# Performance work log

Measured on AMD Instinct MI355X. Metric: run time of the kernel, lower is better.

Reference implementation:

```python
import jax, jax.numpy as jnp
import numpy as np

DIM, ORDER, HID = 512, 2, 64
B, S = 4, 8192


def setup_inputs() -> dict:
    key = jax.random.key(0)
    ks = jax.random.split(key, 16)
    rnd = lambda k, shape, scale: (jax.random.normal(k, shape, dtype=jnp.float32) * scale)
    return {
        'x': rnd(ks[0], (B, S, DIM), 1.0),
        # ImplicitFilter MLP: Linear(1,64) -> GELU -> Linear(64,64) -> GELU -> Linear(64,dim)
        'w1': rnd(ks[1], (1, HID), 1.0),
        'b1': rnd(ks[2], (HID,), 0.02),
        'w2': rnd(ks[3], (HID, HID), 1.0 / np.sqrt(HID)),
        'b2': rnd(ks[4], (HID,), 0.02),
        'w3': rnd(ks[5], (HID, DIM), 1.0 / np.sqrt(HID)),
        'b3': rnd(ks[6], (DIM,), 0.02),
        # depthwise Conv1d(dim, dim, k=3, padding=1, groups=dim): weight (dim, 3)
        'conv_w': rnd(ks[7], (DIM, 3), 1.0 / np.sqrt(3)),
        'conv_b': rnd(ks[8], (DIM,), 0.02),
        # in_proj: Linear(dim, dim*(order+1))
        'w_in': rnd(ks[9], (DIM, DIM * (ORDER + 1)), 1.0 / np.sqrt(DIM)),
        'b_in': rnd(ks[10], (DIM * (ORDER + 1),), 0.02),
        # out_proj: Linear(dim, dim)
        'w_out': rnd(ks[11], (DIM, DIM), 1.0 / np.sqrt(DIM)),
        'b_out': rnd(ks[12], (DIM,), 0.02),
    }


def _gelu(x):
    return jax.nn.gelu(x, approximate=False)  # torch nn.GELU default is exact erf


def reference(x, w1, b1, w2, b2, w3, b3, conv_w, conv_b, w_in, b_in, w_out, b_out):
    batch, seq_len, dim = x.shape
    # in_proj and split into order+1 paths
    proj = x @ w_in + b_in                      # (B, S, 3D)
    v, u, z = jnp.split(proj, 3, axis=-1)       # each (B, S, D)
    # implicit filter from positions
    pos = jnp.linspace(0.0, 1.0, seq_len, dtype=x.dtype)[:, None]   # (S, 1)
    filt = _gelu(_gelu(pos @ w1 + b1) @ w2 + b2) @ w3 + b3          # (S, D)
    # depthwise short conv, kernel=3, padding=1 (cross-correlation as in torch)
    up = jnp.pad(u, ((0, 0), (1, 1), (0, 0)))
    u_short = (up[:, :-2] * conv_w[:, 0] + up[:, 1:-1] * conv_w[:, 1]
               + up[:, 2:] * conv_w[:, 2] + conv_b)                 # (B, S, D)
    # FFT long convolution (circular, matching torch rfft/irfft with n=seq_len)
    U = jnp.fft.rfft(u_short, axis=1)                               # (B, S//2+1, D)
    F = jnp.fft.rfft(filt, n=seq_len, axis=0)[None]                 # (1, S//2+1, D)
    filtered = jnp.fft.irfft(U * F, n=seq_len, axis=1)              # (B, S, D)
    # multiplicative gates
    out = v * filtered * jax.nn.sigmoid(z)
    return out @ w_out + b_out
```

## Files before the change

### kernel.cpp

```cpp
#include <hip/hip_runtime.h>
#include <math.h>

#define DIM   512
#define NB    4
#define NS    8192
#define FFT_N 8192
#define FT    1024
#define MTOT  (NB*NS)

#define IDX(i) ((i) + ((i) >> 3))
#define XSZ   9216

typedef __attribute__((ext_vector_type(8))) short bf16x8;
typedef __attribute__((ext_vector_type(4))) short short4v;
typedef __attribute__((ext_vector_type(8))) short short8v;
typedef __attribute__((ext_vector_type(4))) float f32x4;

__device__ __forceinline__ float bf2f(unsigned short u) {
    union { unsigned int i; float f; } v; v.i = ((unsigned int)u) << 16; return v.f;
}
__device__ __forceinline__ unsigned short f2bf(float f) {
    union { float f; unsigned int i; } v; v.f = f;
    unsigned int r = v.i + 0x7fffu + ((v.i >> 16) & 1u);
    return (unsigned short)(r >> 16);
}
__device__ __forceinline__ float2 cmulf(float2 a, float2 b) {
    return make_float2(a.x*b.x - a.y*b.y, a.x*b.y + a.y*b.x);
}
__device__ __forceinline__ float2 cadd(float2 a, float2 b) { return make_float2(a.x+b.x, a.y+b.y); }
__device__ __forceinline__ float2 csub(float2 a, float2 b) { return make_float2(a.x-b.x, a.y-b.y); }
__device__ __forceinline__ float gelu_exact(float x) {
    return 0.5f * x * (1.0f + erff(x * 0.70710678118654752f));
}
__device__ __forceinline__ void gload16(const void* g, void* l) {
    __builtin_amdgcn_global_load_lds((const __attribute__((address_space(1))) void*)g,
                                     (__attribute__((address_space(3))) void*)l, 16, 0, 0);
}

__global__ void filter_mlp_kernel(const float* __restrict__ w1, const float* __restrict__ b1,
                                  const float* __restrict__ w2, const float* __restrict__ b2,
                                  const float* __restrict__ w3, const float* __restrict__ b3,
                                  float* __restrict__ filt) {
    __shared__ float h1[64];
    __shared__ float h2[64];
    const int s = blockIdx.x;
    const int t = threadIdx.x;
    const float pos = (float)s / (float)(NS - 1);
    h1[t] = gelu_exact(pos * w1[t] + b1[t]);
    __syncthreads();
    float acc = b2[t];
    #pragma unroll 8
    for (int j = 0; j < 64; ++j) acc += h1[j] * w2[j*64 + t];
    h2[t] = gelu_exact(acc);
    __syncthreads();
    for (int d = t; d < DIM; d += 64) {
        float o = b3[d];
        #pragma unroll 8
        for (int j = 0; j < 64; ++j) o += h2[j] * w3[j*DIM + d];
        filt[(size_t)s*DIM + d] = o;
    }
}

__global__ void transpose_f32_kernel(const float* __restrict__ in, float* __restrict__ out,
                                     int R, int C) {
    __shared__ float tile[64][65];
    const int c0 = blockIdx.x * 64, r0 = blockIdx.y * 64;
    const int t = threadIdx.x;
    const int rr = t >> 4, c4 = (t & 15) * 4;
    #pragma unroll
    for (int p = 0; p < 4; ++p) {
        const int r = rr + p*16;
        float4 v = *(const float4*)&in[(size_t)(r0 + r)*C + c0 + c4];
        tile[r][c4+0]=v.x; tile[r][c4+1]=v.y; tile[r][c4+2]=v.z; tile[r][c4+3]=v.w;
    }
    __syncthreads();
    const int cc = t >> 4, r4 = (t & 15) * 4;
    #pragma unroll
    for (int p = 0; p < 4; ++p) {
        const int c = cc + p*16;
        float4 o = make_float4(tile[r4+0][c], tile[r4+1][c], tile[r4+2][c], tile[r4+3][c]);
        *(float4*)&out[(size_t)(c0 + c)*R + r0 + r4] = o;
    }
}

__global__ void castT_kernel(const float* __restrict__ in, unsigned short* __restrict__ outT,
                             int R, int C) {
    __shared__ float tile[64][65];
    const int c0 = blockIdx.x * 64, r0 = blockIdx.y * 64;
    const int t = threadIdx.x;
    const int rr = t >> 4, c4 = (t & 15) * 4;
    #pragma unroll
    for (int p = 0; p < 4; ++p) {
        const int r = rr + p*16;
        float4 v = *(const float4*)&in[(size_t)(r0 + r)*C + c0 + c4];
        tile[r][c4+0]=v.x; tile[r][c4+1]=v.y; tile[r][c4+2]=v.z; tile[r][c4+3]=v.w;
    }
    __syncthreads();
    const int cc = t >> 4, r4 = (t & 15) * 4;
    #pragma unroll
    for (int p = 0; p < 4; ++p) {
        const int c = cc + p*16;
        short4v o;
        o[0] = (short)f2bf(tile[r4+0][c]); o[1] = (short)f2bf(tile[r4+1][c]);
        o[2] = (short)f2bf(tile[r4+2][c]); o[3] = (short)f2bf(tile[r4+3][c]);
        *(short4v*)&outT[(size_t)(c0 + c)*R + r0 + r4] = o;
    }
}

__global__ void cast_x_kernel(const float* __restrict__ in, unsigned short* __restrict__ out) {
    const size_t i = ((size_t)blockIdx.x * 256 + threadIdx.x) * 8;
    float4 a = *(const float4*)&in[i];
    float4 b = *(const float4*)&in[i+4];
    short8v o;
    o[0]=(short)f2bf(a.x); o[1]=(short)f2bf(a.y); o[2]=(short)f2bf(a.z); o[3]=(short)f2bf(a.w);
    o[4]=(short)f2bf(b.x); o[5]=(short)f2bf(b.y); o[6]=(short)f2bf(b.z); o[7]=(short)f2bf(b.w);
    *(short8v*)&out[i] = o;
}

template<int LOGQ>
__device__ __forceinline__ void dif4_stage(float2* X) {
    const int q = 1 << LOGQ;
    const float step = -6.28318530717958647692f / (float)(4*q);
    #pragma unroll
    for (int it = 0; it < (FFT_N/4)/FT; ++it) {
        const int idx = threadIdx.x + it*FT;
        const int g = idx >> LOGQ, k = idx & (q-1);
        const int base = (g << (LOGQ+2)) + k;
        const int i0 = IDX(base), i1 = IDX(base+q), i2 = IDX(base+2*q), i3 = IDX(base+3*q);
        float2 a=X[i0], b=X[i1], c=X[i2], d=X[i3];
        float2 t0=cadd(a,c), t1=csub(a,c), t2=cadd(b,d), t3=csub(b,d);
        float2 y0=cadd(t0,t2), y2=csub(t0,t2);
        float2 y1=make_float2(t1.x+t3.y, t1.y-t3.x);
        float2 y3=make_float2(t1.x-t3.y, t1.y+t3.x);
        float sv, cv; __sincosf(step*(float)k, &sv, &cv);
        float2 w1=make_float2(cv, sv);
        float2 w2=cmulf(w1, w1);
        float2 w3=cmulf(w2, w1);
        X[i0] = y0;
        X[i1] = cmulf(y1, w1);
        X[i2] = cmulf(y2, w2);
        X[i3] = cmulf(y3, w3);
    }
    __syncthreads();
}

template<int LOGQ>
__device__ __forceinline__ void dit4_stage_inv(float2* X) {
    const int q = 1 << LOGQ;
    const float step = 6.28318530717958647692f / (float)(4*q);
    #pragma unroll
    for (int it = 0; it < (FFT_N/4)/FT; ++it) {
        const int idx = threadIdx.x + it*FT;
        const int g = idx >> LOGQ, k = idx & (q-1);
        const int base = (g << (LOGQ+2)) + k;
        const int i0 = IDX(base), i1 = IDX(base+q), i2 = IDX(base+2*q), i3 = IDX(base+3*q);
        float sv, cv; __sincosf(step*(float)k, &sv, &cv);
        float2 w1=make_float2(cv, sv);
        float2 w2=cmulf(w1, w1);
        float2 w3=cmulf(w2, w1);
        float2 u0=X[i0];
        float2 u1=cmulf(X[i1], w1);
        float2 u2=cmulf(X[i2], w2);
        float2 u3=cmulf(X[i3], w3);
        float2 s02=cadd(u0,u2), d02=csub(u0,u2);
        float2 s13=cadd(u1,u3), d13=csub(u1,u3);
        X[i0] = cadd(s02, s13);
        X[i2] = csub(s02, s13);
        X[i1] = make_float2(d02.x - d13.y, d02.y + d13.x);
        X[i3] = make_float2(d02.x + d13.y, d02.y - d13.x);
    }
    __syncthreads();
}

__device__ __forceinline__ void reg_fwd(float2* E) {
    const float C = 0.70710678118654752f;
    {
        float2 t0=cadd(E[0],E[4]), t1=csub(E[0],E[4]);
        float2 t2=cadd(E[2],E[6]), t3=csub(E[2],E[6]);
        E[0]=cadd(t0,t2);
        E[4]=csub(t0,t2);
        E[2]=make_float2(t1.x+t3.y, t1.y-t3.x);
        E[6]=make_float2(t1.x-t3.y, t1.y+t3.x);
    }
    {
        float2 t0=cadd(E[1],E[5]), t1=csub(E[1],E[5]);
        float2 t2=cadd(E[3],E[7]), t3=csub(E[3],E[7]);
        float2 y0=cadd(t0,t2), y2=csub(t0,t2);
        float2 y1=make_float2(t1.x+t3.y, t1.y-t3.x);
        float2 y3=make_float2(t1.x-t3.y, t1.y+t3.x);
        E[1]=y0;
        E[3]=make_float2(C*(y1.x+y1.y),  C*(y1.y-y1.x));
        E[5]=make_float2(y2.y, -y2.x);
        E[7]=make_float2(C*(y3.y-y3.x), -C*(y3.x+y3.y));
    }
    #pragma unroll
    for (int j = 0; j < 8; j += 2) {
        float2 a=E[j], b=E[j+1];
        E[j]=cadd(a,b); E[j+1]=csub(a,b);
    }
}
__device__ __forceinline__ void reg_inv(float2* E) {
    const float C = 0.70710678118654752f;
    #pragma unroll
    for (int j = 0; j < 8; j += 2) {
        float2 a=E[j], b=E[j+1];
        E[j]=cadd(a,b); E[j+1]=csub(a,b);
    }
    {
        float2 u0=E[0], u1=E[2], u2=E[4], u3=E[6];
        float2 s02=cadd(u0,u2), d02=csub(u0,u2);
        float2 s13=cadd(u1,u3), d13=csub(u1,u3);
        E[0]=cadd(s02,s13);
        E[4]=csub(s02,s13);
        E[2]=make_float2(d02.x - d13.y, d02.y + d13.x);
        E[6]=make_float2(d02.x + d13.y, d02.y - d13.x);
    }
    {
        float2 z1=E[3], z2=E[5], z3=E[7];
        float2 u0=E[1];
        float2 u1=make_float2(C*(z1.x - z1.y), C*(z1.x + z1.y));
        float2 u2=make_float2(-z2.y, z2.x);
        float2 u3=make_float2(-C*(z3.x + z3.y), C*(z3.x - z3.y));
        float2 s02=cadd(u0,u2), d02=csub(u0,u2);
        float2 s13=cadd(u1,u3), d13=csub(u1,u3);
        E[1]=cadd(s02,s13);
        E[5]=csub(s02,s13);
        E[3]=make_float2(d02.x - d13.y, d02.y + d13.x);
        E[7]=make_float2(d02.x + d13.y, d02.y - d13.x);
    }
}

__device__ __forceinline__ void load8p(const float2* X, int t, float2* E) {
    const float2* b = X + 9*t;
    #pragma unroll
    for (int j = 0; j < 8; ++j) E[j] = b[j];
}
__device__ __forceinline__ void store8p(float2* X, int t, const float2* E) {
    float2* b = X + 9*t;
    #pragma unroll
    for (int j = 0; j < 8; ++j) b[j] = E[j];
}

__global__ __launch_bounds__(FT)
void fft_filt_kernel(const float* __restrict__ filtT, float2* __restrict__ Fbr) {
    __shared__ float2 X[XSZ];
    const int dd = blockIdx.x;
    const int t = threadIdx.x;
    const float* f = filtT + (size_t)dd * FFT_N;
    {
        float4 a = *(const float4*)(f + 8*t);
        float4 b = *(const float4*)(f + 8*t + 4);
        float2 E[8];
        E[0]=make_float2(a.x,0.f); E[1]=make_float2(a.y,0.f);
        E[2]=make_float2(a.z,0.f); E[3]=make_float2(a.w,0.f);
        E[4]=make_float2(b.x,0.f); E[5]=make_float2(b.y,0.f);
        E[6]=make_float2(b.z,0.f); E[7]=make_float2(b.w,0.f);
        store8p(X, t, E);
    }
    __syncthreads();
    dif4_stage<11>(X);
    dif4_stage<9>(X);
    dif4_stage<7>(X);
    dif4_stage<5>(X);
    dif4_stage<3>(X);
    {
        float2 E[8];
        load8p(X, t, E);
        reg_fwd(E);
        float2* o = Fbr + (size_t)dd*FFT_N + 8*t;
        #pragma unroll
        for (int j = 0; j < 8; ++j) o[j] = E[j];
    }
}

__global__ __launch_bounds__(FT)
void fft_conv_kernel(unsigned short* __restrict__ uT, const float2* __restrict__ Fbr) {
    __shared__ float2 X[XSZ];
    const int d = blockIdx.x & (DIM - 1);
    const int p = blockIdx.x >> 9;
    unsigned short* u1 = uT + (size_t)((2*p    )*DIM + d) * FFT_N;
    unsigned short* u2 = uT + (size_t)((2*p + 1)*DIM + d) * FFT_N;
    const int t = threadIdx.x;
    {
        short8v a = *(const short8v*)(u1 + 8*t);
        short8v b = *(const short8v*)(u2 + 8*t);
        float2 E[8];
        #pragma unroll
        for (int j = 0; j < 8; ++j)
            E[j] = make_float2(bf2f((unsigned short)a[j]), bf2f((unsigned short)b[j]));
        store8p(X, t, E);
    }
    __syncthreads();
    dif4_stage<11>(X);
    dif4_stage<9>(X);
    dif4_stage<7>(X);
    dif4_stage<5>(X);
    dif4_stage<3>(X);
    {
        float2 E[8];
        load8p(X, t, E);
        reg_fwd(E);
        const float2* F = Fbr + (size_t)d*FFT_N + 8*t;
        #pragma unroll
        for (int j = 0; j < 8; ++j) E[j] = cmulf(E[j], F[j]);
        reg_inv(E);
        store8p(X, t, E);
    }
    __syncthreads();
    dit4_stage_inv<3>(X);
    dit4_stage_inv<5>(X);
    dit4_stage_inv<7>(X);
    dit4_stage_inv<9>(X);
    dit4_stage_inv<11>(X);
    {
        float2 E[8];
        load8p(X, t, E);
        const float sc = 1.0f / (float)FFT_N;
        short8v a, b;
        #pragma unroll
        for (int j = 0; j < 8; ++j) {
            a[j] = (short)f2bf(E[j].x * sc);
            b[j] = (short)f2bf(E[j].y * sc);
        }
        *(short8v*)(u1 + 8*t) = a;
        *(short8v*)(u2 + 8*t) = b;
    }
}

__global__ void conv_transpose_kernel(const unsigned short* __restrict__ u,
                                      const float* __restrict__ conv_w,
                                      const float* __restrict__ conv_b,
                                      unsigned short* __restrict__ uT) {
    __shared__ float tile[66][65];
    const int bid = blockIdx.x;
    const int dt = bid & 7, st = (bid >> 3) & 127, b = bid >> 10;
    const int d0 = dt*64, s0 = st*64;
    const int t = threadIdx.x;
    const int rr = t >> 4, c4 = (t & 15) * 4;
    for (int r = rr; r < 66; r += 16) {
        const int s = s0 + r - 1;
        float v0=0.f, v1=0.f, v2=0.f, v3=0.f;
        if (s >= 0 && s < NS) {
            short4v xv = *(const short4v*)&u[((size_t)(b*NS + s))*DIM + d0 + c4];
            v0=bf2f((unsigned short)xv[0]); v1=bf2f((unsigned short)xv[1]);
            v2=bf2f((unsigned short)xv[2]); v3=bf2f((unsigned short)xv[3]);
        }
        tile[r][c4]=v0; tile[r][c4+1]=v1; tile[r][c4+2]=v2; tile[r][c4+3]=v3;
    }
    __syncthreads();
    const int dl = t >> 4, s4 = (t & 15) * 4;
    #pragma unroll
    for (int p = 0; p < 4; ++p) {
        const int dc = dl + p*16;
        const int d = d0 + dc;
        const float w0 = conv_w[d*3], w1 = conv_w[d*3+1], w2 = conv_w[d*3+2];
        const float cb = conv_b[d];
        short4v o;
        #pragma unroll
        for (int j = 0; j < 4; ++j) {
            const int sx = s4 + j;
            const float val = tile[sx][dc]*w0 + tile[sx+1][dc]*w1 + tile[sx+2][dc]*w2 + cb;
            o[j] = (short)f2bf(val);
        }
        *(short4v*)&uT[((size_t)(b*DIM + d))*FFT_N + s0 + s4] = o;
    }
}

template<int MODE>
__global__ __launch_bounds__(256)
void gemm_bt_kernel(const unsigned short* __restrict__ A,
                    const unsigned short* __restrict__ BT,
                    const float* __restrict__ bias,
                    float* __restrict__ Cf,
                    unsigned short* __restrict__ Cb) {
    __shared__ unsigned short As[2][4096];
    __shared__ unsigned short Bs[2][4096];
    const int tid = threadIdx.x;
    const int wid = tid >> 6, lane = tid & 63;
    const int bid = blockIdx.y * 4 + blockIdx.x;
    const int swz = (bid & 7) * 128 + (bid >> 3);
    const int m0 = (swz >> 2) * 128, n0 = (swz & 3) * 128;
    const int srow = wid*16 + (lane >> 2);
    const int scol = (lane & 3) * 8;
    const unsigned short* gA = A  + (size_t)(m0 + srow)*DIM + scol;
    const unsigned short* gB = BT + (size_t)(n0 + srow)*DIM + scol;
    const int wr = wid >> 1, wc = wid & 1;
    const int fr = lane & 15, fq = lane >> 4;
    f32x4 acc[4][4] = {};
    gload16(gA,                  &As[0][wid*512]);
    gload16(gA + (size_t)64*DIM, &As[0][wid*512 + 2048]);
    gload16(gB,                  &Bs[0][wid*512]);
    gload16(gB + (size_t)64*DIM, &Bs[0][wid*512 + 2048]);
    int cur = 0;
    for (int k0 = 0; k0 < DIM; k0 += 32) {
        __syncthreads();
        if (k0 + 32 < DIM) {
            const int nx = cur ^ 1;
            gload16(gA + k0 + 32,                  &As[nx][wid*512]);
            gload16(gA + k0 + 32 + (size_t)64*DIM, &As[nx][wid*512 + 2048]);
            gload16(gB + k0 + 32,                  &Bs[nx][wid*512]);
            gload16(gB + k0 + 32 + (size_t)64*DIM, &Bs[nx][wid*512 + 2048]);
        }
        bf16x8 af[4], bfr[4];
        #pragma unroll
        for (int mi = 0; mi < 4; ++mi)
            af[mi] = *(const bf16x8*)&As[cur][(wr*64 + mi*16 + fr)*32 + fq*8];
        #pragma unroll
        for (int ni = 0; ni < 4; ++ni)
            bfr[ni] = *(const bf16x8*)&Bs[cur][(wc*64 + ni*16 + fr)*32 + fq*8];
        #pragma unroll
        for (int mi = 0; mi < 4; ++mi)
            #pragma unroll
            for (int ni = 0; ni < 4; ++ni)
                acc[mi][ni] = __builtin_amdgcn_mfma_f32_16x16x32_bf16(af[mi], bfr[ni], acc[mi][ni], 0, 0, 0);
        cur ^= 1;
    }
    #pragma unroll
    for (int ni = 0; ni < 4; ++ni) {
        const int c = n0 + wc*64 + ni*16 + fr;
        const float bv = bias[c];
        #pragma unroll
        for (int mi = 0; mi < 4; ++mi) {
            const int rbase = m0 + wr*64 + mi*16 + fq*4;
            #pragma unroll
            for (int j = 0; j < 4; ++j) {
                const size_t idx = (size_t)(rbase + j)*DIM + c;
                const float val = acc[mi][ni][j] + bv;
                if (MODE == 0) Cb[idx] = f2bf(val);
                else           Cf[idx] = val;
            }
        }
    }
}

__global__ __launch_bounds__(256)
void gemm_vzg_kernel(const unsigned short* __restrict__ A,
                     const unsigned short* __restrict__ BT,
                     const float* __restrict__ bias,
                     const unsigned short* __restrict__ yT,
                     unsigned short* __restrict__ Cb) {
    __shared__ unsigned short As[2][4096];
    __shared__ unsigned short Bv[2][4096];
    __shared__ unsigned short Bz[2][4096];
    const int tid = threadIdx.x;
    const int wid = tid >> 6, lane = tid & 63;
    const int bid = blockIdx.y * 4 + blockIdx.x;
    const int swz = (bid & 7) * 128 + (bid >> 3);
    const int m0 = (swz >> 2) * 128, n0 = (swz & 3) * 128;
    const int srow = wid*16 + (lane >> 2);
    const int scol = (lane & 3) * 8;
    const unsigned short* gA  = A  + (size_t)(m0 + srow)*DIM + scol;
    const unsigned short* gBv = BT + (size_t)(n0 + srow)*DIM + scol;
    const unsigned short* gBz = BT + (size_t)(1024 + n0 + srow)*DIM + scol;
    const int wr = wid >> 1, wc = wid & 1;
    const int fr = lane & 15, fq = lane >> 4;
    f32x4 accv[4][4] = {};
    f32x4 accz[4][4] = {};
    gload16(gA,                   &As[0][wid*512]);
    gload16(gA  + (size_t)64*DIM, &As[0][wid*512 + 2048]);
    gload16(gBv,                  &Bv[0][wid*512]);
    gload16(gBv + (size_t)64*DIM, &Bv[0][wid*512 + 2048]);
    gload16(gBz,                  &Bz[0][wid*512]);
    gload16(gBz + (size_t)64*DIM, &Bz[0][wid*512 + 2048]);
    int cur = 0;
    for (int k0 = 0; k0 < DIM; k0 += 32) {
        __syncthreads();
        if (k0 + 32 < DIM) {
            const int nx = cur ^ 1;
            gload16(gA  + k0 + 32,                  &As[nx][wid*512]);
            gload16(gA  + k0 + 32 + (size_t)64*DIM, &As[nx][wid*512 + 2048]);
            gload16(gBv + k0 + 32,                  &Bv[nx][wid*512]);
            gload16(gBv + k0 + 32 + (size_t)64*DIM, &Bv[nx][wid*512 + 2048]);
            gload16(gBz + k0 + 32,                  &Bz[nx][wid*512]);
            gload16(gBz + k0 + 32 + (size_t)64*DIM, &Bz[nx][wid*512 + 2048]);
        }
        bf16x8 af[4], bf_[4];
        #pragma unroll
        for (int mi = 0; mi < 4; ++mi)
            af[mi] = *(const bf16x8*)&As[cur][(wr*64 + mi*16 + fr)*32 + fq*8];
        #pragma unroll
        for (int ni = 0; ni < 4; ++ni)
            bf_[ni] = *(const bf16x8*)&Bv[cur][(wc*64 + ni*16 + fr)*32 + fq*8];
        #pragma unroll
        for (int mi = 0; mi < 4; ++mi)
            #pragma unroll
            for (int ni = 0; ni < 4; ++ni)
                accv[mi][ni] = __builtin_amdgcn_mfma_f32_16x16x32_bf16(af[mi], bf_[ni], accv[mi][ni], 0, 0, 0);
        #pragma unroll
        for (int ni = 0; ni < 4; ++ni)
            bf_[ni] = *(const bf16x8*)&Bz[cur][(wc*64 + ni*16 + fr)*32 + fq*8];
        #pragma unroll
        for (int mi = 0; mi < 4; ++mi)
            #pragma unroll
            for (int ni = 0; ni < 4; ++ni)
                accz[mi][ni] = __builtin_amdgcn_mfma_f32_16x16x32_bf16(af[mi], bf_[ni], accz[mi][ni], 0, 0, 0);
        cur ^= 1;
    }
    const int b    = m0 >> 13;
    const int srel = (m0 & (NS-1)) + wr*64;
    #pragma unroll
    for (int ni = 0; ni < 4; ++ni) {
        const int c = n0 + wc*64 + ni*16 + fr;
        const float bv = bias[c];
        const float bz = bias[1024 + c];
        const unsigned short* yrow = yT + ((size_t)(b*DIM + c))*FFT_N + srel;
        #pragma unroll
        for (int mi = 0; mi < 4; ++mi) {
            const short4v yv = *(const short4v*)&yrow[mi*16 + fq*4];
            const int rbase = m0 + wr*64 + mi*16 + fq*4;
            #pragma unroll
            for (int j = 0; j < 4; ++j) {
                const size_t idx = (size_t)(rbase + j)*DIM + c;
                const float vv = accv[mi][ni][j] + bv;
                const float zz = accz[mi][ni][j] + bz;
                const float sg = 1.0f / (1.0f + __expf(-zz));
                const float yf = bf2f((unsigned short)yv[j]);
                Cb[idx] = f2bf(vv * sg * yf);
            }
        }
    }
}

extern "C" void kernel_launch(void* const* d_in, const int* in_sizes, int n_in,
                              void* d_out, int out_size, void* d_ws, size_t ws_size,
                              hipStream_t stream) {
    const float* x      = (const float*)d_in[0];
    const float* w1     = (const float*)d_in[1];
    const float* b1     = (const float*)d_in[2];
    const float* w2     = (const float*)d_in[3];
    const float* b2     = (const float*)d_in[4];
    const float* w3     = (const float*)d_in[5];
    const float* b3     = (const float*)d_in[6];
    const float* conv_w = (const float*)d_in[7];
    const float* conv_b = (const float*)d_in[8];
    const float* w_in   = (const float*)d_in[9];
    const float* b_in   = (const float*)d_in[10];
    const float* w_out  = (const float*)d_in[11];
    const float* b_out  = (const float*)d_in[12];
    float* out = (float*)d_out;

    const size_t NEED = 167772160ULL;
    if (ws_size < NEED) return;
    char* ws = (char*)d_ws;
    float2*         Fbr    = (float2*)ws;
    unsigned short* xb     = (unsigned short*)(ws + (size_t)( 32<<20));
    unsigned short* W2     = (unsigned short*)(ws + (size_t)( 64<<20));
    unsigned short* W3     = (unsigned short*)(ws + (size_t)( 96<<20));
    char*           W4     = ws + (size_t)(128<<20);
    float*          filt   = (float*)W4;
    float*          filtT  = (float*)(ws + (size_t)(96<<20));
    unsigned short* w_inT  = (unsigned short*)W4;
    unsigned short* w_outT = (unsigned short*)(W4 + (size_t)(2<<20));

    filter_mlp_kernel<<<NS, 64, 0, stream>>>(w1, b1, w2, b2, w3, b3, filt);
    transpose_f32_kernel<<<dim3(DIM/64, NS/64), 256, 0, stream>>>(filt, filtT, NS, DIM);
    fft_filt_kernel<<<DIM, FT, 0, stream>>>(filtT, Fbr);
    cast_x_kernel<<<(MTOT*DIM/8)/256, 256, 0, stream>>>(x, xb);
    castT_kernel<<<dim3(1536/64, DIM/64), 256, 0, stream>>>(w_in, w_inT, DIM, 1536);
    castT_kernel<<<dim3(DIM/64, DIM/64), 256, 0, stream>>>(w_out, w_outT, DIM, DIM);
    gemm_bt_kernel<0><<<dim3(4, MTOT/128), 256, 0, stream>>>(xb, w_inT + 512*DIM, b_in + 512, nullptr, W2);
    conv_transpose_kernel<<<NB*(NS/64)*(DIM/64), 256, 0, stream>>>(W2, conv_w, conv_b, W3);
    fft_conv_kernel<<<(NB/2)*DIM, FT, 0, stream>>>(W3, Fbr);
    gemm_vzg_kernel<<<dim3(4, MTOT/128), 256, 0, stream>>>(xb, w_inT, b_in, W3, W2);
    gemm_bt_kernel<2><<<dim3(4, MTOT/128), 256, 0, stream>>>(W2, w_outT, b_out, out, nullptr);
}
```

Measured before the change: 269.1 us.

## Compute v, u, z projections in one GEMM and apply FFT gate separately

```diff
diff --git a/kernel.cpp b/kernel.cpp
--- a/kernel.cpp
+++ b/kernel.cpp
@@ -363,6 +363,35 @@
             o[j] = (short)f2bf(val);
         }
         *(short4v*)&uT[((size_t)(b*DIM + d))*FFT_N + s0 + s4] = o;
+    }
+}
+
+__global__ void gate_kernel(unsigned short* __restrict__ vg, const unsigned short* __restrict__ yT) {
+    __shared__ float tile[64][65];
+    const int bid = blockIdx.x;
+    const int dt = bid & 7, st = (bid >> 3) & 127, b = bid >> 10;
+    const int d0 = dt*64, s0 = st*64;
+    const int t = threadIdx.x;
+    const int dl = t >> 4, s4 = (t & 15) * 4;
+    #pragma unroll
+    for (int p = 0; p < 4; ++p) {
+        const int d = dl + p*16;
+        short4v y = *(const short4v*)&yT[((size_t)(b*DIM + d0 + d))*FFT_N + s0 + s4];
+        tile[d][s4]  =bf2f((unsigned short)y[0]); tile[d][s4+1]=bf2f((unsigned short)y[1]);
+        tile[d][s4+2]=bf2f((unsigned short)y[2]); tile[d][s4+3]=bf2f((unsigned short)y[3]);
+    }
+    __syncthreads();
+    const int sl = t >> 4, d4 = (t & 15) * 4;
+    #pragma unroll
+    for (int p = 0; p < 4; ++p) {
+        const int s = s0 + sl + p*16;
+        unsigned short* pv = &vg[((size_t)(b*NS + s))*DIM + d0 + d4];
+        short4v v = *(short4v*)pv;
+        short4v o;
+        #pragma unroll
+        for (int j = 0; j < 4; ++j)
+            o[j] = (short)f2bf(bf2f((unsigned short)v[j]) * tile[d4+j][sl + p*16]);
+        *(short4v*)pv = o;
     }
 }
 
@@ -434,13 +463,14 @@
 }
 
 __global__ __launch_bounds__(256)
-void gemm_vzg_kernel(const unsigned short* __restrict__ A,
+void gemm_vzu_kernel(const unsigned short* __restrict__ A,
                      const unsigned short* __restrict__ BT,
                      const float* __restrict__ bias,
-                     const unsigned short* __restrict__ yT,
-                     unsigned short* __restrict__ Cb) {
+                     unsigned short* __restrict__ Gb,
+                     unsigned short* __restrict__ Ub) {
     __shared__ unsigned short As[2][4096];
     __shared__ unsigned short Bv[2][4096];
+    __shared__ unsigned short Bu[2][4096];
     __shared__ unsigned short Bz[2][4096];
     const int tid = threadIdx.x;
     const int wid = tid >> 6, lane = tid & 63;
@@ -451,15 +481,19 @@
     const int scol = (lane & 3) * 8;
     const unsigned short* gA  = A  + (size_t)(m0 + srow)*DIM + scol;
     const unsigned short* gBv = BT + (size_t)(n0 + srow)*DIM + scol;
+    const unsigned short* gBu = BT + (size_t)(512  + n0 + srow)*DIM + scol;
     const unsigned short* gBz = BT + (size_t)(1024 + n0 + srow)*DIM + scol;
     const int wr = wid >> 1, wc = wid & 1;
     const int fr = lane & 15, fq = lane >> 4;
     f32x4 accv[4][4] = {};
+    f32x4 accu[4][4] = {};
     f32x4 accz[4][4] = {};
     gload16(gA,                   &As[0][wid*512]);
     gload16(gA  + (size_t)64*DIM, &As[0][wid*512 + 2048]);
     gload16(gBv,                  &Bv[0][wid*512]);
     gload16(gBv + (size_t)64*DIM, &Bv[0][wid*512 + 2048]);
+    gload16(gBu,                  &Bu[0][wid*512]);
+    gload16(gBu + (size_t)64*DIM, &Bu[0][wid*512 + 2048]);
     gload16(gBz,                  &Bz[0][wid*512]);
     gload16(gBz + (size_t)64*DIM, &Bz[0][wid*512 + 2048]);
     int cur = 0;
@@ -471,6 +505,8 @@
             gload16(gA  + k0 + 32 + (size_t)64*DIM, &As[nx][wid*512 + 2048]);
             gload16(gBv + k0 + 32,                  &Bv[nx][wid*512]);
             gload16(gBv + k0 + 32 + (size_t)64*DIM, &Bv[nx][wid*512 + 2048]);
+            gload16(gBu + k0 + 32,                  &Bu[nx][wid*512]);
+            gload16(gBu + k0 + 32 + (size_t)64*DIM, &Bu[nx][wid*512 + 2048]);
             gload16(gBz + k0 + 32,                  &Bz[nx][wid*512]);
             gload16(gBz + k0 + 32 + (size_t)64*DIM, &Bz[nx][wid*512 + 2048]);
         }
@@ -486,6 +522,14 @@
             #pragma unroll
             for (int ni = 0; ni < 4; ++ni)
                 accv[mi][ni] = __builtin_amdgcn_mfma_f32_16x16x32_bf16(af[mi], bf_[ni], accv[mi][ni], 0, 0, 0);
+        #pragma unroll
+        for (int ni = 0; ni < 4; ++ni)
+            bf_[ni] = *(const bf16x8*)&Bu[cur][(wc*64 + ni*16 + fr)*32 + fq*8];
+        #pragma unroll
+        for (int mi = 0; mi < 4; ++mi)
+            #pragma unroll
+            for (int ni = 0; ni < 4; ++ni)
+                accu[mi][ni] = __builtin_amdgcn_mfma_f32_16x16x32_bf16(af[mi], bf_[ni], accu[mi][ni], 0, 0, 0);
         #pragma unroll
         for (int ni = 0; ni < 4; ++ni)
             bf_[ni] = *(const bf16x8*)&Bz[cur][(wc*64 + ni*16 + fr)*32 + fq*8];
@@ -496,26 +540,24 @@
                 accz[mi][ni] = __builtin_amdgcn_mfma_f32_16x16x32_bf16(af[mi], bf_[ni], accz[mi][ni], 0, 0, 0);
         cur ^= 1;
     }
-    const int b    = m0 >> 13;
-    const int srel = (m0 & (NS-1)) + wr*64;
     #pragma unroll
     for (int ni = 0; ni < 4; ++ni) {
         const int c = n0 + wc*64 + ni*16 + fr;
         const float bv = bias[c];
+        const float bu = bias[512  + c];
         const float bz = bias[1024 + c];
-        const unsigned short* yrow = yT + ((size_t)(b*DIM + c))*FFT_N + srel;
         #pragma unroll
         for (int mi = 0; mi < 4; ++mi) {
-            const short4v yv = *(const short4v*)&yrow[mi*16 + fq*4];
             const int rbase = m0 + wr*64 + mi*16 + fq*4;
             #pragma unroll
             for (int j = 0; j < 4; ++j) {
                 const size_t idx = (size_t)(rbase + j)*DIM + c;
                 const float vv = accv[mi][ni][j] + bv;
+                const float uu = accu[mi][ni][j] + bu;
                 const float zz = accz[mi][ni][j] + bz;
                 const float sg = 1.0f / (1.0f + __expf(-zz));
-                const float yf = bf2f((unsigned short)yv[j]);
-                Cb[idx] = f2bf(vv * sg * yf);
+                Gb[idx] = f2bf(vv * sg);
+                Ub[idx] = f2bf(uu);
             }
         }
     }
@@ -558,9 +600,9 @@
     cast_x_kernel<<<(MTOT*DIM/8)/256, 256, 0, stream>>>(x, xb);
     castT_kernel<<<dim3(1536/64, DIM/64), 256, 0, stream>>>(w_in, w_inT, DIM, 1536);
     castT_kernel<<<dim3(DIM/64, DIM/64), 256, 0, stream>>>(w_out, w_outT, DIM, DIM);
-    gemm_bt_kernel<0><<<dim3(4, MTOT/128), 256, 0, stream>>>(xb, w_inT + 512*DIM, b_in + 512, nullptr, W2);
-    conv_transpose_kernel<<<NB*(NS/64)*(DIM/64), 256, 0, stream>>>(W2, conv_w, conv_b, W3);
-    fft_conv_kernel<<<(NB/2)*DIM, FT, 0, stream>>>(W3, Fbr);
-    gemm_vzg_kernel<<<dim3(4, MTOT/128), 256, 0, stream>>>(xb, w_inT, b_in, W3, W2);
+    gemm_vzu_kernel<<<dim3(4, MTOT/128), 256, 0, stream>>>(xb, w_inT, b_in, W2, W3);
+    conv_transpose_kernel<<<NB*(NS/64)*(DIM/64), 256, 0, stream>>>(W3, conv_w, conv_b, xb);
+    fft_conv_kernel<<<(NB/2)*DIM, FT, 0, stream>>>(xb, Fbr);
+    gate_kernel<<<NB*(NS/64)*(DIM/64), 256, 0, stream>>>(W2, xb);
     gemm_bt_kernel<2><<<dim3(4, MTOT/128), 256, 0, stream>>>(W2, w_outT, b_out, out, nullptr);
 }
```

After: 299.9 us. 1.11x slower.
